# Kernel tuning notes

Hardware: AMD Instinct MI355X
Metric: run time of the kernel (lower is better)

Reference implementation:

```python
import jax, jax.numpy as jnp
import numpy as np

B, K, H, W = 16, 64, 160, 160
EPS = 1e-5


def setup_inputs() -> dict:
    key = jax.random.key(0)
    k1, k2 = jax.random.split(key)
    # keypoints[..., 0] = x in [0, W-1], keypoints[..., 1] = y in [0, H-1]
    kp = jax.random.uniform(k1, (B, K, 2), dtype=jnp.float32)
    keypoints = kp * jnp.array([W - 1.0, H - 1.0], dtype=jnp.float32)
    DetectionMap = jax.random.uniform(k2, (B, K, H, W), dtype=jnp.float32)
    return {
        "keypoints": keypoints,
        "reconDetectionMap_std_x": jnp.float32(6.0),
        "reconDetectionMap_std_y": jnp.float32(6.0),
        "correlation": jnp.float32(0.1),
        "DetectionMap": DetectionMap,
    }


def reference(keypoints, reconDetectionMap_std_x, reconDetectionMap_std_y, correlation, DetectionMap):
    sx = reconDetectionMap_std_x
    sy = reconDetectionMap_std_y
    rho = correlation
    Bv, Kv, Hv, Wv = DetectionMap.shape

    one_m_rho2 = 1.0 - rho * rho
    den = 1.0 / (2.0 * jnp.pi * sx * sy * jnp.sqrt(one_m_rho2))
    num1 = -1.0 / (2.0 * one_m_rho2)

    ii = jnp.arange(Hv, dtype=keypoints.dtype)  # rows (y)
    jj = jnp.arange(Wv, dtype=keypoints.dtype)  # cols (x)
    # dy: [B,K,H,1], dx: [B,K,1,W] -> broadcast to [B,K,H,W] only inside num2
    dy = ii[None, None, :, None] - keypoints[:, :, 1][:, :, None, None]
    dx = jj[None, None, None, :] - keypoints[:, :, 0][:, :, None, None]

    num2 = (dy * dy) / (sy * sy) + (dx * dx) / (sx * sx) \
        - (2.0 * rho / (sx * sy)) * dy * dx  # [B,K,H,W]
    scoreMap = den * jnp.exp(num1 * num2)  # [B,K,H,W]

    denom = jnp.sum(scoreMap, axis=1, keepdims=True) + EPS  # [B,1,H,W]
    return scoreMap / denom
```

## Files before the change

kernel.cpp:

```cpp
#include <hip/hip_runtime.h>

#define KK 64
#define HH 160
#define WW 160
#define HWPIX (HH * WW)
#define EPSF 1e-5f

__global__ __launch_bounds__(256) void recon_confmap_kernel(
    const float* __restrict__ kp,
    const float* __restrict__ sx_p,
    const float* __restrict__ sy_p,
    const float* __restrict__ rho_p,
    float* __restrict__ out)
{
    __shared__ float2 skp[KK];

    const int b   = blockIdx.y;
    const int tid = threadIdx.x;

    if (tid < KK) {
        skp[tid] = ((const float2*)(kp + (size_t)b * KK * 2))[tid];
    }

    const float sx  = sx_p[0];
    const float sy  = sy_p[0];
    const float rho = rho_p[0];
    __syncthreads();

    const float L2E   = 1.44269504088896340736f;
    const float omr2  = 1.0f - rho * rho;
    const float num1  = -0.5f / omr2;
    const float ca    = num1 / (sy * sy) * L2E;
    const float cb    = num1 / (sx * sx) * L2E;
    const float cc    = num1 * (-2.0f * rho / (sx * sy)) * L2E;
    const float epsod = EPSF * (2.0f * 3.14159265358979323846f * sx * sy * sqrtf(omr2));

    const int p  = blockIdx.x * 256 + tid;
    const int i  = p / WW;
    const int j  = p - i * WW;
    const float fi = (float)i;
    const float fj = (float)j;

    float s[KK];
    float sum = 0.0f;
#pragma unroll
    for (int k = 0; k < KK; ++k) {
        const float dy  = fi - skp[k].y;
        const float dx  = fj - skp[k].x;
        const float arg = fmaf(ca * dy, dy, fmaf(cb * dx, dx, cc * dy * dx));
        const float e   = __builtin_amdgcn_exp2f(arg);
        s[k] = e;
        sum += e;
    }

    const float inv = 1.0f / (sum + epsod);

    float* op = out + (size_t)b * KK * HWPIX + p;
#pragma unroll
    for (int k = 0; k < KK; ++k) {
        op[(size_t)k * HWPIX] = s[k] * inv;
    }
}

extern "C" void kernel_launch(void* const* d_in, const int* in_sizes, int n_in,
                              void* d_out, int out_size, void* d_ws, size_t ws_size,
                              hipStream_t stream) {
    const float* kp    = (const float*)d_in[0];
    const float* sx_p  = (const float*)d_in[1];
    const float* sy_p  = (const float*)d_in[2];
    const float* rho_p = (const float*)d_in[3];
    float* out = (float*)d_out;

    const int B = in_sizes[0] / (KK * 2);
    dim3 grid(HWPIX / 256, B);
    recon_confmap_kernel<<<grid, 256, 0, stream>>>(kp, sx_p, sy_p, rho_p, out);
}
```

Before: 169.8 us.

## Process four pixels per thread with float4 stores and recompute exps instead of caching

Each thread now handles four horizontally adjacent pixels, using finite differences along x to get the exponent arguments cheaply. The 64-entry register array is dropped: exponentials are recomputed in a second pass, which cuts register pressure. Output is written as float4 vector stores, and blocks shrink to 64 threads. The cost is doubled exp work, in exchange for wider stores and higher occupancy on a kernel that is bound by output writes. The incremental differences add a small floating-point rounding deviation.

Measured after the change: 174.7 us. 1.03x slower.

```diff
diff --git a/kernel.cpp b/kernel.cpp
--- a/kernel.cpp
+++ b/kernel.cpp
@@ -6,7 +6,7 @@
 #define HWPIX (HH * WW)
 #define EPSF 1e-5f
 
-__global__ __launch_bounds__(256) void recon_confmap_kernel(
+__global__ __launch_bounds__(64) void recon_confmap_kernel(
     const float* __restrict__ kp,
     const float* __restrict__ sx_p,
     const float* __restrict__ sy_p,
@@ -18,9 +18,7 @@
     const int b   = blockIdx.y;
     const int tid = threadIdx.x;
 
-    if (tid < KK) {
-        skp[tid] = ((const float2*)(kp + (size_t)b * KK * 2))[tid];
-    }
+    skp[tid] = ((const float2*)(kp + (size_t)b * KK * 2))[tid];
 
     const float sx  = sx_p[0];
     const float sy  = sy_p[0];
@@ -33,32 +31,60 @@
     const float ca    = num1 / (sy * sy) * L2E;
     const float cb    = num1 / (sx * sx) * L2E;
     const float cc    = num1 * (-2.0f * rho / (sx * sy)) * L2E;
+    const float c2b   = 2.0f * cb;
     const float epsod = EPSF * (2.0f * 3.14159265358979323846f * sx * sy * sqrtf(omr2));
 
-    const int p  = blockIdx.x * 256 + tid;
-    const int i  = p / WW;
-    const int j  = p - i * WW;
+    const int P  = (blockIdx.x * 64 + tid) * 4;
+    const int i  = P / WW;
+    const int j0 = P - i * WW;
     const float fi = (float)i;
-    const float fj = (float)j;
+    const float fj = (float)j0;
 
-    float s[KK];
-    float sum = 0.0f;
+    float s0 = 0.f, s1 = 0.f, s2 = 0.f, s3 = 0.f;
 #pragma unroll
     for (int k = 0; k < KK; ++k) {
         const float dy  = fi - skp[k].y;
         const float dx  = fj - skp[k].x;
-        const float arg = fmaf(ca * dy, dy, fmaf(cb * dx, dx, cc * dy * dx));
-        const float e   = __builtin_amdgcn_exp2f(arg);
-        s[k] = e;
-        sum += e;
+        const float tA  = cc * dy;
+        const float tyy = ca * dy * dy;
+        const float a0  = fmaf(tA, dx, fmaf(cb * dx, dx, tyy));
+        float d = fmaf(c2b, dx, tA) + cb;
+        const float a1 = a0 + d; d += c2b;
+        const float a2 = a1 + d; d += c2b;
+        const float a3 = a2 + d;
+        s0 += __builtin_amdgcn_exp2f(a0);
+        s1 += __builtin_amdgcn_exp2f(a1);
+        s2 += __builtin_amdgcn_exp2f(a2);
+        s3 += __builtin_amdgcn_exp2f(a3);
     }
 
-    const float inv = 1.0f / (sum + epsod);
+    const float i0 = 1.0f / (s0 + epsod);
+    const float i1 = 1.0f / (s1 + epsod);
+    const float i2 = 1.0f / (s2 + epsod);
+    const float i3 = 1.0f / (s3 + epsod);
 
-    float* op = out + (size_t)b * KK * HWPIX + p;
+    float fi2 = fi, fj2 = fj;
+    asm("" : "+v"(fi2), "+v"(fj2));
+
+    float* op = out + (size_t)b * KK * HWPIX + P;
+
 #pragma unroll
     for (int k = 0; k < KK; ++k) {
-        op[(size_t)k * HWPIX] = s[k] * inv;
+        const float dy  = fi2 - skp[k].y;
+        const float dx  = fj2 - skp[k].x;
+        const float tA  = cc * dy;
+        const float tyy = ca * dy * dy;
+        const float a0  = fmaf(tA, dx, fmaf(cb * dx, dx, tyy));
+        float d = fmaf(c2b, dx, tA) + cb;
+        const float a1 = a0 + d; d += c2b;
+        const float a2 = a1 + d; d += c2b;
+        const float a3 = a2 + d;
+        float4 v;
+        v.x = __builtin_amdgcn_exp2f(a0) * i0;
+        v.y = __builtin_amdgcn_exp2f(a1) * i1;
+        v.z = __builtin_amdgcn_exp2f(a2) * i2;
+        v.w = __builtin_amdgcn_exp2f(a3) * i3;
+        *(float4*)(op + (size_t)k * HWPIX) = v;
     }
 }
 
@@ -72,6 +98,6 @@
     float* out = (float*)d_out;
 
     const int B = in_sizes[0] / (KK * 2);
-    dim3 grid(HWPIX / 256, B);
-    recon_confmap_kernel<<<grid, 256, 0, stream>>>(kp, sx_p, sy_p, rho_p, out);
+    dim3 grid(HWPIX / (64 * 4), B);
+    recon_confmap_kernel<<<grid, 64, 0, stream>>>(kp, sx_p, sy_p, rho_p, out);
 }
```
